# Performance work log

Hardware: AMD Instinct MI355X
Metric: run time of the kernel (lower is better)

## Reference

```python
import jax, jax.numpy as jnp
import numpy as np


def setup_inputs() -> dict:
    key = jax.random.key(0)
    kq, kk, kv = jax.random.split(key, 3)
    B, S, H, D = 1, 4096, 16, 64
    q = jax.random.normal(kq, (B, S, H, D), dtype=jnp.float32)
    k = jax.random.normal(kk, (B, S, H, D), dtype=jnp.float32)
    v = jax.random.normal(kv, (B, S, H, D), dtype=jnp.float32)
    return {"q": q, "k": k, "v": v, "causal": 1}


def reference(q, k, v, causal):
    B, S, H, D = q.shape
    scale = D ** (-0.5)
    # scores: [B, H, S_q, S_k]
    scores = jnp.einsum("bqhd,bkhd->bhqk", q, k) * scale
    if causal:
        mask = jnp.triu(jnp.ones((S, S), dtype=bool), k=1)  # True above diagonal
        scores = jnp.where(mask, -jnp.inf, scores)
    attn = jax.nn.softmax(scores, axis=-1)
    out = jnp.einsum("bhqk,bkhd->bqhd", attn, v)
    return out
```

## Files before the change

### kernel.cpp

```cpp
#include <hip/hip_runtime.h>
#include <stdint.h>

#define S_LEN 4096
#define NH    16
#define HD    64
#define RSTR  (NH * HD)

typedef __attribute__((ext_vector_type(8))) __bf16 bf16x8;
typedef __attribute__((ext_vector_type(4))) short short4v;
typedef __attribute__((ext_vector_type(4))) float floatx4;

union BF4 { unsigned short u[4]; unsigned d[2]; short4v s; };

__device__ __forceinline__ unsigned pkbf(float a, float b) {
    unsigned ua = __builtin_bit_cast(unsigned, a) + 0x8000u;
    unsigned ub = __builtin_bit_cast(unsigned, b) + 0x8000u;
    return __builtin_amdgcn_perm(ub, ua, 0x07060302u);
}

__device__ __forceinline__ floatx4 mfma16(short4v a, short4v b, floatx4 c) {
#if __has_builtin(__builtin_amdgcn_mfma_f32_16x16x16bf16_1k)
    return __builtin_amdgcn_mfma_f32_16x16x16bf16_1k(a, b, c, 0, 0, 0);
#else
    floatx4 d;
    asm volatile("v_mfma_f32_16x16x16_bf16 %0, %1, %2, %3\n\ts_nop 7\n\ts_nop 7"
                 : "=v"(d) : "v"(a), "v"(b), "v"(c));
    return d;
#endif
}

__device__ __forceinline__ void gl16(const void* g, void* l) {
#if __has_builtin(__builtin_amdgcn_global_load_lds)
    __builtin_amdgcn_global_load_lds((const __attribute__((address_space(1))) unsigned int*)g,
                                     (__attribute__((address_space(3))) unsigned int*)l, 16, 0, 0);
#else
    *(uint4*)l = *(const uint4*)g;
#endif
}

__global__ __launch_bounds__(256)
void pp_kv(const float* __restrict__ K, const float* __restrict__ V,
           unsigned short* __restrict__ Kz, unsigned short* __restrict__ Vz) {
    __shared__ __align__(16) float vt[64][68];
    const int bid = blockIdx.x;
    const int h   = bid & 15;
    const int tau = bid >> 4;
    const int tid = threadIdx.x;
    {
        const int r = tid >> 2, gg = tid & 3;
        const float* kp = K + ((size_t)(64 * tau + r) * NH + h) * HD + 16 * gg;
        const float4 a = *reinterpret_cast<const float4*>(kp);
        const float4 b = *reinterpret_cast<const float4*>(kp + 4);
        const float4 c = *reinterpret_cast<const float4*>(kp + 8);
        const float4 d = *reinterpret_cast<const float4*>(kp + 12);
        uint4 f0, f1;
        f0.x = pkbf(a.x, a.y); f0.y = pkbf(a.z, a.w);
        f0.z = pkbf(b.x, b.y); f0.w = pkbf(b.z, b.w);
        f1.x = pkbf(c.x, c.y); f1.y = pkbf(c.z, c.w);
        f1.z = pkbf(d.x, d.y); f1.w = pkbf(d.z, d.w);
        unsigned short* out = Kz + ((size_t)(h * 64 + tau)) * 4096 + r * 64;
        *reinterpret_cast<uint4*>(out + (((2 * gg)     ^ (r & 7)) * 8)) = f0;
        *reinterpret_cast<uint4*>(out + (((2 * gg + 1) ^ (r & 7)) * 8)) = f1;
    }
    {
        const int r = tid >> 2, ch = tid & 3;
        const float* vrow = V + ((size_t)(64 * tau + r) * NH + h) * HD + 4 * ch;
        #pragma unroll
        for (int k2 = 0; k2 < 4; ++k2)
            *reinterpret_cast<float4*>(&vt[r][4 * ch + 16 * k2]) =
                *reinterpret_cast<const float4*>(vrow + 16 * k2);
    }
    __syncthreads();
    {
        const int dr = tid & 63, kg = tid >> 6;
        float x[16];
        #pragma unroll
        for (int j = 0; j < 16; ++j) x[j] = vt[16 * kg + j][dr];
        uint4 g0, g1;
        g0.x = pkbf(x[0],  x[1]);  g0.y = pkbf(x[2],  x[3]);
        g0.z = pkbf(x[4],  x[5]);  g0.w = pkbf(x[6],  x[7]);
        g1.x = pkbf(x[8],  x[9]);  g1.y = pkbf(x[10], x[11]);
        g1.z = pkbf(x[12], x[13]); g1.w = pkbf(x[14], x[15]);
        unsigned short* out = Vz + ((size_t)(h * 64 + tau)) * 4096 + dr * 64;
        *reinterpret_cast<uint4*>(out + (((2 * kg)     ^ (dr & 7)) * 8)) = g0;
        *reinterpret_cast<uint4*>(out + (((2 * kg + 1) ^ (dr & 7)) * 8)) = g1;
    }
}

__global__ __launch_bounds__(256, 3)
void fa_main(const float* __restrict__ Q, const unsigned short* __restrict__ Kz,
             const unsigned short* __restrict__ Vz, const int* __restrict__ causal_p,
             float* __restrict__ O) {
    __shared__ __align__(16) unsigned char smem[49152];
    unsigned short* Klds = (unsigned short*)smem;
    unsigned short* Vlds = (unsigned short*)(smem + 24576);
    unsigned short* Qlds = (unsigned short*)(smem + 16384);
    float* Lred = (float*)smem;
    float* Lsum = (float*)(smem + 18432);

    const int bid = blockIdx.x;
    const int h   = bid & 15;
    const int x   = 63 - (bid >> 4);
    const int q0  = x * 64;

    const int tid = threadIdx.x;
    const int wv  = tid >> 6;
    const int wq  = wv & 1;
    const int wk  = wv >> 1;
    const int ln  = tid & 63;
    const int c16 = ln & 15;
    const int qd  = ln >> 4;
    const int causal = causal_p[0];

    const float SC = 0.18033688011112042f;

    const char* kg = (const char*)Kz + (size_t)h * 64 * 8192 + wv * 2048 + ln * 16;
    const char* vg = (const char*)Vz + (size_t)h * 64 * 8192 + wv * 2048 + ln * 16;
    char* kl = (char*)smem + wv * 2048 + ln * 16;
    char* vl = (char*)smem + 24576 + wv * 2048 + ln * 16;

#define GLDS_TILE(IT, BUF) do {                                  \
    const char* ks_ = kg + (size_t)(IT) * 8192;                  \
    const char* vs_ = vg + (size_t)(IT) * 8192;                  \
    char* kd_ = kl + (BUF) * 8192;                               \
    char* vd_ = vl + (BUF) * 8192;                               \
    gl16(ks_, kd_); gl16(ks_ + 1024, kd_ + 1024);                \
    gl16(vs_, vd_); gl16(vs_ + 1024, vd_ + 1024);                \
} while (0)

    GLDS_TILE(0, 0);
    GLDS_TILE(1, 1);

    {
        const int r = tid >> 2, gg = tid & 3;
        const float* qp = Q + ((size_t)(q0 + r) * NH + h) * HD + 16 * gg;
        const float4 a = *reinterpret_cast<const float4*>(qp);
        const float4 b = *reinterpret_cast<const float4*>(qp + 4);
        const float4 c = *reinterpret_cast<const float4*>(qp + 8);
        const float4 d = *reinterpret_cast<const float4*>(qp + 12);
        uint4 f0, f1;
        f0.x = pkbf(a.x * SC, a.y * SC); f0.y = pkbf(a.z * SC, a.w * SC);
        f0.z = pkbf(b.x * SC, b.y * SC); f0.w = pkbf(b.z * SC, b.w * SC);
        f1.x = pkbf(c.x * SC, c.y * SC); f1.y = pkbf(c.z * SC, c.w * SC);
        f1.z = pkbf(d.x * SC, d.y * SC); f1.w = pkbf(d.z * SC, d.w * SC);
        unsigned short* out = Qlds + r * 64;
        *reinterpret_cast<uint4*>(out + (((2 * gg)     ^ (r & 7)) * 8)) = f0;
        *reinterpret_cast<uint4*>(out + (((2 * gg + 1) ^ (r & 7)) * 8)) = f1;
    }

    const int nIter = causal ? (x + 1) : (S_LEN / 64);

    floatx4 acc[4][2];
    #pragma unroll
    for (int m = 0; m < 4; ++m)
        #pragma unroll
        for (int t = 0; t < 2; ++t) acc[m][t] = floatx4{0.f, 0.f, 0.f, 0.f};
    float lacc[2] = {0.f, 0.f};

    const int e7 = c16 & 7;
    const int o0 = (qd ^ e7) * 8;
    const int o1 = ((4 + qd) ^ e7) * 8;
    const int vo0 = ((4 * wk + 0 + (qd >> 1)) ^ e7) * 8 + (qd & 1) * 4;
    const int vo1 = ((4 * wk + 2 + (qd >> 1)) ^ e7) * 8 + (qd & 1) * 4;

    __syncthreads();

    bf16x8 qh0[2], qh1[2];
    #pragma unroll
    for (int t = 0; t < 2; ++t) {
        const unsigned short* qrow = Qlds + (16 * (2 * wq + t) + c16) * 64;
        qh0[t] = *reinterpret_cast<const bf16x8*>(qrow + o0);
        qh1[t] = *reinterpret_cast<const bf16x8*>(qrow + o1);
    }
    __syncthreads();

    int br = 0;
    int b2 = 2;
    for (int it = 0; it < nIter; ++it) {
        if (it == nIter - 1) {
            asm volatile("s_waitcnt vmcnt(0)" ::: "memory");
        } else {
            asm volatile("s_waitcnt vmcnt(4)" ::: "memory");
        }
        __builtin_amdgcn_s_barrier();

        if (it + 2 < nIter) GLDS_TILE(it + 2, b2);

        const unsigned short* Kb = Klds + br * 4096;
        const unsigned short* Vb = Vlds + br * 4096;

        bf16x8 kf0[2], kf1[2];
        #pragma unroll
        for (int ks = 0; ks < 2; ++ks) {
            const unsigned short* krow = Kb + (32 * wk + 16 * ks + c16) * 64;
            kf0[ks] = *reinterpret_cast<const bf16x8*>(krow + o0);
            kf1[ks] = *reinterpret_cast<const bf16x8*>(krow + o1);
        }

        const bool maskit = (causal != 0) && (it == nIter - 1);

        BF4 pf[2][2];
        #pragma unroll
        for (int ks = 0; ks < 2; ++ks) {
            const int kvb = 32 * wk + 16 * ks + 4 * qd;
            #pragma unroll
            for (int t = 0; t < 2; ++t) {
                floatx4 st = __builtin_amdgcn_mfma_f32_16x16x32_bf16(
                    kf0[ks], qh0[t], floatx4{0.f, 0.f, 0.f, 0.f}, 0, 0, 0);
                st = __builtin_amdgcn_mfma_f32_16x16x32_bf16(kf1[ks], qh1[t], st, 0, 0, 0);
                const int qloc = 16 * (2 * wq + t) + c16;
                float p[4];
                #pragma unroll
                for (int i = 0; i < 4; ++i) {
                    float sv = st[i];
                    if (maskit && (kvb + i > qloc)) sv = -1e30f;
                    p[i] = __builtin_amdgcn_exp2f(sv);
                }
                lacc[t] += (p[0] + p[1]) + (p[2] + p[3]);
                pf[ks][t].d[0] = pkbf(p[0], p[1]);
                pf[ks][t].d[1] = pkbf(p[2], p[3]);
            }
        }

        #pragma unroll
        for (int md = 0; md < 4; ++md) {
            const unsigned short* vrow = Vb + (16 * md + c16) * 64;
            BF4 vf0, vf1;
            *reinterpret_cast<uint2*>(&vf0.d[0]) = *reinterpret_cast<const uint2*>(vrow + vo0);
            *reinterpret_cast<uint2*>(&vf1.d[0]) = *reinterpret_cast<const uint2*>(vrow + vo1);
            #pragma unroll
            for (int t = 0; t < 2; ++t) {
                acc[md][t] = mfma16(vf0.s, pf[0][t].s, acc[md][t]);
                acc[md][t] = mfma16(vf1.s, pf[1][t].s, acc[md][t]);
            }
        }

        br = (br == 2) ? 0 : br + 1;
        b2 = (b2 == 2) ? 0 : b2 + 1;
    }

    __syncthreads();

    #pragma unroll
    for (int t = 0; t < 2; ++t) {
        float lt = lacc[t];
        lt += __shfl_xor(lt, 16);
        lt += __shfl_xor(lt, 32);
        if (qd == 0) Lsum[wk * 64 + wq * 32 + t * 16 + c16] = lt;
    }
    if (wk == 0) {
        float* Lw = Lred + (wq * 64 + ln) * 36;
        #pragma unroll
        for (int md = 0; md < 4; ++md)
            #pragma unroll
            for (int t = 0; t < 2; ++t)
                *reinterpret_cast<floatx4*>(&Lw[(md * 2 + t) * 4]) = acc[md][t];
    }
    __syncthreads();
    if (wk == 1) {
        const float* Lr = Lred + (wq * 64 + ln) * 36;
        float inv[2];
        #pragma unroll
        for (int t = 0; t < 2; ++t) {
            const int qidx = wq * 32 + t * 16 + c16;
            inv[t] = 1.0f / (Lsum[qidx] + Lsum[64 + qidx]);
        }
        #pragma unroll
        for (int md = 0; md < 4; ++md)
            #pragma unroll
            for (int t = 0; t < 2; ++t) {
                const floatx4 b = *reinterpret_cast<const floatx4*>(&Lr[(md * 2 + t) * 4]);
                const floatx4 a = acc[md][t];
                floatx4 o;
                o[0] = (a[0] + b[0]) * inv[t];
                o[1] = (a[1] + b[1]) * inv[t];
                o[2] = (a[2] + b[2]) * inv[t];
                o[3] = (a[3] + b[3]) * inv[t];
                const int q = q0 + 16 * (2 * wq + t) + c16;
                *reinterpret_cast<floatx4*>(O + ((size_t)q * NH + h) * HD + 16 * md + 4 * qd) = o;
            }
    }
}

extern "C" void kernel_launch(void* const* d_in, const int* in_sizes, int n_in,
                              void* d_out, int out_size, void* d_ws, size_t ws_size,
                              hipStream_t stream) {
    const float* q = (const float*)d_in[0];
    const float* k = (const float*)d_in[1];
    const float* v = (const float*)d_in[2];
    const int* causal = (const int*)d_in[3];
    float* out = (float*)d_out;
    unsigned short* Kz = (unsigned short*)d_ws;
    unsigned short* Vz = Kz + (size_t)NH * 64 * 4096;
    pp_kv<<<dim3(64 * NH), dim3(256), 0, stream>>>(k, v, Kz, Vz);
    fa_main<<<dim3(64 * NH), dim3(256), 0, stream>>>(q, Kz, Vz, causal, out);
}
```

Measured before the change: 142.3 us.

## Shrink V staging to two LDS buffers for four blocks per CU and reorder tiles

```diff
diff --git a/kernel.cpp b/kernel.cpp
--- a/kernel.cpp
+++ b/kernel.cpp
@@ -87,11 +87,11 @@
     }
 }
 
-__global__ __launch_bounds__(256, 3)
+__global__ __launch_bounds__(256, 4)
 void fa_main(const float* __restrict__ Q, const unsigned short* __restrict__ Kz,
              const unsigned short* __restrict__ Vz, const int* __restrict__ causal_p,
              float* __restrict__ O) {
-    __shared__ __align__(16) unsigned char smem[49152];
+    __shared__ __align__(16) unsigned char smem[40960];
     unsigned short* Klds = (unsigned short*)smem;
     unsigned short* Vlds = (unsigned short*)(smem + 24576);
     unsigned short* Qlds = (unsigned short*)(smem + 16384);
@@ -100,7 +100,14 @@
 
     const int bid = blockIdx.x;
     const int h   = bid & 15;
-    const int x   = 63 - (bid >> 4);
+    const int r4  = bid >> 4;
+    const int sl  = r4 >> 4;
+    const int g4  = r4 & 15;
+    int x;
+    if      (sl == 0) x = 2 * g4;
+    else if (sl == 1) x = 2 * g4 + 1;
+    else if (sl == 2) x = 62 - 2 * g4;
+    else              x = 63 - 2 * g4;
     const int q0  = x * 64;
 
     const int tid = threadIdx.x;
@@ -119,17 +126,22 @@
     char* kl = (char*)smem + wv * 2048 + ln * 16;
     char* vl = (char*)smem + 24576 + wv * 2048 + ln * 16;
 
-#define GLDS_TILE(IT, BUF) do {                                  \
+#define GK_TILE(IT, BUF) do {                                    \
     const char* ks_ = kg + (size_t)(IT) * 8192;                  \
+    char* kd_ = kl + (BUF) * 8192;                               \
+    gl16(ks_, kd_); gl16(ks_ + 1024, kd_ + 1024);                \
+} while (0)
+#define GV_TILE(IT, BUF) do {                                    \
     const char* vs_ = vg + (size_t)(IT) * 8192;                  \
-    char* kd_ = kl + (BUF) * 8192;                               \
     char* vd_ = vl + (BUF) * 8192;                               \
-    gl16(ks_, kd_); gl16(ks_ + 1024, kd_ + 1024);                \
     gl16(vs_, vd_); gl16(vs_ + 1024, vd_ + 1024);                \
 } while (0)
 
-    GLDS_TILE(0, 0);
-    GLDS_TILE(1, 1);
+    const int nIter = causal ? (x + 1) : (S_LEN / 64);
+
+    GV_TILE(0, 0);
+    GK_TILE(0, 0);
+    if (nIter > 1) GK_TILE(1, 1);
 
     {
         const int r = tid >> 2, gg = tid & 3;
@@ -148,8 +160,6 @@
         *reinterpret_cast<uint4*>(out + (((2 * gg + 1) ^ (r & 7)) * 8)) = f1;
     }
 
-    const int nIter = causal ? (x + 1) : (S_LEN / 64);
-
     floatx4 acc[4][2];
     #pragma unroll
     for (int m = 0; m < 4; ++m)
@@ -174,20 +184,21 @@
     }
     __syncthreads();
 
-    int br = 0;
-    int b2 = 2;
+    int kbr = 0;
+    int kb2 = 2;
     for (int it = 0; it < nIter; ++it) {
-        if (it == nIter - 1) {
+        if (it + 1 < nIter) {
+            asm volatile("s_waitcnt vmcnt(2)" ::: "memory");
+        } else {
             asm volatile("s_waitcnt vmcnt(0)" ::: "memory");
-        } else {
-            asm volatile("s_waitcnt vmcnt(4)" ::: "memory");
         }
         __builtin_amdgcn_s_barrier();
 
-        if (it + 2 < nIter) GLDS_TILE(it + 2, b2);
-
-        const unsigned short* Kb = Klds + br * 4096;
-        const unsigned short* Vb = Vlds + br * 4096;
+        if (it + 1 < nIter) GV_TILE(it + 1, (it + 1) & 1);
+        if (it + 2 < nIter) GK_TILE(it + 2, kb2);
+
+        const unsigned short* Kb = Klds + kbr * 4096;
+        const unsigned short* Vb = Vlds + (it & 1) * 4096;
 
         bf16x8 kf0[2], kf1[2];
         #pragma unroll
@@ -235,8 +246,8 @@
             }
         }
 
-        br = (br == 2) ? 0 : br + 1;
-        b2 = (b2 == 2) ? 0 : b2 + 1;
+        kbr = (kbr == 2) ? 0 : kbr + 1;
+        kb2 = (kb2 == 2) ? 0 : kb2 + 1;
     }
 
     __syncthreads();
```

Measured after the change: 150.5 us. 5.8% more time.

## Double query tile per block to 128 rows and reorder causal block schedule

Applied to the files above, without the earlier changes.

```diff
diff --git a/kernel.cpp b/kernel.cpp
--- a/kernel.cpp
+++ b/kernel.cpp
@@ -87,21 +87,22 @@
     }
 }
 
-__global__ __launch_bounds__(256, 3)
+__global__ __launch_bounds__(256, 2)
 void fa_main(const float* __restrict__ Q, const unsigned short* __restrict__ Kz,
              const unsigned short* __restrict__ Vz, const int* __restrict__ causal_p,
              float* __restrict__ O) {
     __shared__ __align__(16) unsigned char smem[49152];
     unsigned short* Klds = (unsigned short*)smem;
     unsigned short* Vlds = (unsigned short*)(smem + 24576);
-    unsigned short* Qlds = (unsigned short*)(smem + 16384);
+    unsigned short* Qlds = (unsigned short*)(smem + 8192);
     float* Lred = (float*)smem;
-    float* Lsum = (float*)(smem + 18432);
+    float* Lsum = (float*)(smem + 34816);
 
     const int bid = blockIdx.x;
     const int h   = bid & 15;
-    const int x   = 63 - (bid >> 4);
-    const int q0  = x * 64;
+    const int r4  = bid >> 4;
+    const int x   = (r4 < 16) ? (31 - r4) : (r4 - 16);
+    const int q0  = x * 128;
 
     const int tid = threadIdx.x;
     const int wv  = tid >> 6;
@@ -129,50 +130,56 @@
 } while (0)
 
     GLDS_TILE(0, 0);
-    GLDS_TILE(1, 1);
 
     {
-        const int r = tid >> 2, gg = tid & 3;
-        const float* qp = Q + ((size_t)(q0 + r) * NH + h) * HD + 16 * gg;
-        const float4 a = *reinterpret_cast<const float4*>(qp);
-        const float4 b = *reinterpret_cast<const float4*>(qp + 4);
-        const float4 c = *reinterpret_cast<const float4*>(qp + 8);
-        const float4 d = *reinterpret_cast<const float4*>(qp + 12);
-        uint4 f0, f1;
-        f0.x = pkbf(a.x * SC, a.y * SC); f0.y = pkbf(a.z * SC, a.w * SC);
-        f0.z = pkbf(b.x * SC, b.y * SC); f0.w = pkbf(b.z * SC, b.w * SC);
-        f1.x = pkbf(c.x * SC, c.y * SC); f1.y = pkbf(c.z * SC, c.w * SC);
-        f1.z = pkbf(d.x * SC, d.y * SC); f1.w = pkbf(d.z * SC, d.w * SC);
+        const int r = tid >> 1, hf = tid & 1;
+        const float* qp = Q + ((size_t)(q0 + r) * NH + h) * HD + 32 * hf;
         unsigned short* out = Qlds + r * 64;
-        *reinterpret_cast<uint4*>(out + (((2 * gg)     ^ (r & 7)) * 8)) = f0;
-        *reinterpret_cast<uint4*>(out + (((2 * gg + 1) ^ (r & 7)) * 8)) = f1;
-    }
-
-    const int nIter = causal ? (x + 1) : (S_LEN / 64);
-
-    floatx4 acc[4][2];
+        #pragma unroll
+        for (int cc = 0; cc < 2; ++cc) {
+            const float4 a = *reinterpret_cast<const float4*>(qp + 16 * cc);
+            const float4 b = *reinterpret_cast<const float4*>(qp + 16 * cc + 4);
+            const float4 c = *reinterpret_cast<const float4*>(qp + 16 * cc + 8);
+            const float4 d = *reinterpret_cast<const float4*>(qp + 16 * cc + 12);
+            uint4 f0, f1;
+            f0.x = pkbf(a.x * SC, a.y * SC); f0.y = pkbf(a.z * SC, a.w * SC);
+            f0.z = pkbf(b.x * SC, b.y * SC); f0.w = pkbf(b.z * SC, b.w * SC);
+            f1.x = pkbf(c.x * SC, c.y * SC); f1.y = pkbf(c.z * SC, c.w * SC);
+            f1.z = pkbf(d.x * SC, d.y * SC); f1.w = pkbf(d.z * SC, d.w * SC);
+            const int g = 4 * hf + 2 * cc;
+            *reinterpret_cast<uint4*>(out + (((g)     ^ (r & 7)) * 8)) = f0;
+            *reinterpret_cast<uint4*>(out + (((g + 1) ^ (r & 7)) * 8)) = f1;
+        }
+    }
+
+    const int nIter = causal ? (2 * x + 2) : (S_LEN / 64);
+
+    floatx4 acc[4][4];
     #pragma unroll
     for (int m = 0; m < 4; ++m)
         #pragma unroll
-        for (int t = 0; t < 2; ++t) acc[m][t] = floatx4{0.f, 0.f, 0.f, 0.f};
-    float lacc[2] = {0.f, 0.f};
+        for (int t = 0; t < 4; ++t) acc[m][t] = floatx4{0.f, 0.f, 0.f, 0.f};
+    float lacc[4] = {0.f, 0.f, 0.f, 0.f};
 
     const int e7 = c16 & 7;
     const int o0 = (qd ^ e7) * 8;
     const int o1 = ((4 + qd) ^ e7) * 8;
     const int vo0 = ((4 * wk + 0 + (qd >> 1)) ^ e7) * 8 + (qd & 1) * 4;
     const int vo1 = ((4 * wk + 2 + (qd >> 1)) ^ e7) * 8 + (qd & 1) * 4;
-
-    __syncthreads();
-
-    bf16x8 qh0[2], qh1[2];
+    const int mA = 32 * wk + 4 * qd - 64 * wq - c16;
+
+    __syncthreads();
+
+    bf16x8 qh0[4], qh1[4];
     #pragma unroll
-    for (int t = 0; t < 2; ++t) {
-        const unsigned short* qrow = Qlds + (16 * (2 * wq + t) + c16) * 64;
+    for (int t = 0; t < 4; ++t) {
+        const unsigned short* qrow = Qlds + (64 * wq + 16 * t + c16) * 64;
         qh0[t] = *reinterpret_cast<const bf16x8*>(qrow + o0);
         qh1[t] = *reinterpret_cast<const bf16x8*>(qrow + o1);
     }
     __syncthreads();
+
+    GLDS_TILE(1, 1);
 
     int br = 0;
     int b2 = 2;
@@ -197,23 +204,22 @@
             kf1[ks] = *reinterpret_cast<const bf16x8*>(krow + o1);
         }
 
-        const bool maskit = (causal != 0) && (it == nIter - 1);
-
-        BF4 pf[2][2];
+        const bool mk = (causal != 0) && (it >= nIter - 2);
+        const int rel = (it == nIter - 1) ? 64 : 0;
+
+        BF4 pf[2][4];
         #pragma unroll
         for (int ks = 0; ks < 2; ++ks) {
-            const int kvb = 32 * wk + 16 * ks + 4 * qd;
             #pragma unroll
-            for (int t = 0; t < 2; ++t) {
+            for (int t = 0; t < 4; ++t) {
                 floatx4 st = __builtin_amdgcn_mfma_f32_16x16x32_bf16(
                     kf0[ks], qh0[t], floatx4{0.f, 0.f, 0.f, 0.f}, 0, 0, 0);
                 st = __builtin_amdgcn_mfma_f32_16x16x32_bf16(kf1[ks], qh1[t], st, 0, 0, 0);
-                const int qloc = 16 * (2 * wq + t) + c16;
                 float p[4];
                 #pragma unroll
                 for (int i = 0; i < 4; ++i) {
                     float sv = st[i];
-                    if (maskit && (kvb + i > qloc)) sv = -1e30f;
+                    if (mk && (mA + 16 * ks + i + rel > 16 * t)) sv = -1e30f;
                     p[i] = __builtin_amdgcn_exp2f(sv);
                 }
                 lacc[t] += (p[0] + p[1]) + (p[2] + p[3]);
@@ -229,7 +235,7 @@
             *reinterpret_cast<uint2*>(&vf0.d[0]) = *reinterpret_cast<const uint2*>(vrow + vo0);
             *reinterpret_cast<uint2*>(&vf1.d[0]) = *reinterpret_cast<const uint2*>(vrow + vo1);
             #pragma unroll
-            for (int t = 0; t < 2; ++t) {
+            for (int t = 0; t < 4; ++t) {
                 acc[md][t] = mfma16(vf0.s, pf[0][t].s, acc[md][t]);
                 acc[md][t] = mfma16(vf1.s, pf[1][t].s, acc[md][t]);
             }
@@ -242,41 +248,41 @@
     __syncthreads();
 
     #pragma unroll
-    for (int t = 0; t < 2; ++t) {
+    for (int t = 0; t < 4; ++t) {
         float lt = lacc[t];
         lt += __shfl_xor(lt, 16);
         lt += __shfl_xor(lt, 32);
-        if (qd == 0) Lsum[wk * 64 + wq * 32 + t * 16 + c16] = lt;
+        if (qd == 0) Lsum[wk * 128 + wq * 64 + t * 16 + c16] = lt;
     }
     if (wk == 0) {
-        float* Lw = Lred + (wq * 64 + ln) * 36;
+        float* Lw = Lred + (wq * 64 + ln) * 68;
         #pragma unroll
         for (int md = 0; md < 4; ++md)
             #pragma unroll
-            for (int t = 0; t < 2; ++t)
-                *reinterpret_cast<floatx4*>(&Lw[(md * 2 + t) * 4]) = acc[md][t];
+            for (int t = 0; t < 4; ++t)
+                *reinterpret_cast<floatx4*>(&Lw[(md * 4 + t) * 4]) = acc[md][t];
     }
     __syncthreads();
     if (wk == 1) {
-        const float* Lr = Lred + (wq * 64 + ln) * 36;
-        float inv[2];
-        #pragma unroll
-        for (int t = 0; t < 2; ++t) {
-            const int qidx = wq * 32 + t * 16 + c16;
-            inv[t] = 1.0f / (Lsum[qidx] + Lsum[64 + qidx]);
+        const float* Lr = Lred + (wq * 64 + ln) * 68;
+        float inv[4];
+        #pragma unroll
+        for (int t = 0; t < 4; ++t) {
+            const int qidx = wq * 64 + t * 16 + c16;
+            inv[t] = 1.0f / (Lsum[qidx] + Lsum[128 + qidx]);
         }
         #pragma unroll
         for (int md = 0; md < 4; ++md)
             #pragma unroll
-            for (int t = 0; t < 2; ++t) {
-                const floatx4 b = *reinterpret_cast<const floatx4*>(&Lr[(md * 2 + t) * 4]);
+            for (int t = 0; t < 4; ++t) {
+                const floatx4 b = *reinterpret_cast<const floatx4*>(&Lr[(md * 4 + t) * 4]);
                 const floatx4 a = acc[md][t];
                 floatx4 o;
                 o[0] = (a[0] + b[0]) * inv[t];
                 o[1] = (a[1] + b[1]) * inv[t];
                 o[2] = (a[2] + b[2]) * inv[t];
                 o[3] = (a[3] + b[3]) * inv[t];
-                const int q = q0 + 16 * (2 * wq + t) + c16;
+                const int q = q0 + wq * 64 + 16 * t + c16;
                 *reinterpret_cast<floatx4*>(O + ((size_t)q * NH + h) * HD + 16 * md + 4 * qd) = o;
             }
     }
@@ -293,5 +299,5 @@
     unsigned short* Kz = (unsigned short*)d_ws;
     unsigned short* Vz = Kz + (size_t)NH * 64 * 4096;
     pp_kv<<<dim3(64 * NH), dim3(256), 0, stream>>>(k, v, Kz, Vz);
-    fa_main<<<dim3(64 * NH), dim3(256), 0, stream>>>(q, Kz, Vz, causal, out);
-}
+    fa_main<<<dim3(32 * NH), dim3(256), 0, stream>>>(q, Kz, Vz, causal, out);
+}
```

Result: slower. 159.1 us (+11.8%).
